# Kernel optimization log

Measured on AMD Instinct MI355X. Metric: run time of the kernel, lower is better.

Reference implementation:

```python
import jax, jax.numpy as jnp
import numpy as np

B, S, D, H = 4, 4096, 1024, 64


def setup_inputs() -> dict:
    key = jax.random.key(0)
    k1, k2, k3, k4 = jax.random.split(key, 4)
    x = jax.random.normal(k1, (B, S, D), dtype=jnp.float32)
    # nn.Linear(D, H, bias=False) weights, stored as [D, H] for x @ W
    scale = 1.0 / np.sqrt(D)
    Wk = jax.random.uniform(k2, (D, H), dtype=jnp.float32, minval=-scale, maxval=scale)
    Wq = jax.random.uniform(k3, (D, H), dtype=jnp.float32, minval=-scale, maxval=scale)
    Wv = jax.random.uniform(k4, (D, H), dtype=jnp.float32, minval=-scale, maxval=scale)
    return {"x": x, "Wq": Wq, "Wk": Wk, "Wv": Wv}


def reference(x, Wq, Wk, Wv):
    # x: [B, S, D]
    head_size = Wq.shape[-1]
    q = jnp.einsum('bsd,dh->bsh', x, Wq)
    k = jnp.einsum('bsd,dh->bsh', x, Wk)
    v = jnp.einsum('bsd,dh->bsh', x, Wv)
    scores = jnp.einsum('bqh,bkh->bqk', q, k) * (head_size ** -0.5)  # [B,S,S]
    S_ = x.shape[1]
    causal = jnp.tril(jnp.ones((S_, S_), dtype=bool))
    scores = jnp.where(causal[None, :, :], scores, -jnp.inf)
    attn = jax.nn.softmax(scores, axis=-1)
    return jnp.einsum('bqk,bkh->bqh', attn, v)  # [B,S,H]
```

## Files before the change

kernel.cpp:

```cpp
#include <hip/hip_runtime.h>

typedef __attribute__((ext_vector_type(8))) short bf16x8;
typedef __attribute__((ext_vector_type(4))) short bf16x4;
typedef __attribute__((ext_vector_type(4))) float f32x4;

#define MFMA16(A, Bv, C) __builtin_amdgcn_mfma_f32_16x16x32_bf16((A), (Bv), (C), 0, 0, 0)

static constexpr int NB = 4, NS = 4096, ND = 1024, NH = 64;

__device__ __forceinline__ unsigned short f2bf(float f) {
    union { float f; unsigned int u; } x; x.f = f;
    unsigned int r = x.u + 0x7fffu + ((x.u >> 16) & 1u);
    return (unsigned short)(r >> 16);
}

__device__ __forceinline__ void gload_lds16(const void* g, void* l) {
    __builtin_amdgcn_global_load_lds((const __attribute__((address_space(1))) void*)g,
                                     (__attribute__((address_space(3))) void*)l, 16, 0, 0);
}

__global__ __launch_bounds__(256) void wconv(
    const float* __restrict__ Wq, const float* __restrict__ Wk,
    const float* __restrict__ Wv, unsigned short* __restrict__ wT)
{
    int mn = blockIdx.x;
    int m = mn >> 6, n = mn & 63;
    const float* W = (m == 0) ? Wq : (m == 1) ? Wk : Wv;
    unsigned short* dst = wT + (size_t)mn * ND;
    for (int k = threadIdx.x; k < ND; k += 256)
        dst[k] = f2bf(W[(size_t)k * NH + n]);
}

__global__ __launch_bounds__(512) void qkv_proj(
    const float* __restrict__ x, const unsigned short* __restrict__ wT,
    unsigned short* __restrict__ qo, unsigned short* __restrict__ ko,
    unsigned short* __restrict__ vt)
{
    __shared__ unsigned short Ws[2][192][64];
    __shared__ unsigned short Xs[2][32][72];
    __shared__ unsigned short Ls[32][72];

    const int tid  = threadIdx.x;
    const int lane = tid & 63;
    const int w    = tid >> 6;
    const int lr   = lane & 15;
    const int lg   = lane >> 4;
    const int mg   = w >> 2;
    const int cg   = w & 3;
    const int mbase = blockIdx.x * 32;

    const int wr8 = lane >> 3;
    const int wck = (lane & 7) ^ wr8;
    const int xrow = tid & 31;
    const int xcg  = tid >> 5;

    f32x4 acc[3];
    #pragma unroll
    for (int f = 0; f < 3; ++f) acc[f] = (f32x4){0.f, 0.f, 0.f, 0.f};

    const float* xsrc = x + (size_t)(mbase + xrow) * ND + xcg * 4;

    #define STAGE_W(buf, kb)                                                         \
        do {                                                                         \
            _Pragma("unroll")                                                        \
            for (int i_ = 0; i_ < 3; ++i_) {                                         \
                int rb_ = w * 24 + i_ * 8;                                           \
                gload_lds16(wT + (size_t)(rb_ + wr8) * ND + (kb) + wck * 8,          \
                            &Ws[buf][rb_][0]);                                       \
            }                                                                        \
        } while (0)

    #define LOADX(kb) do { xr = *(const float4*)(xsrc + (kb)); } while (0)

    #define WRITEX(buf)                                                              \
        do {                                                                         \
            bf16x4 p_;                                                               \
            p_[0] = (short)f2bf(xr.x); p_[1] = (short)f2bf(xr.y);                    \
            p_[2] = (short)f2bf(xr.z); p_[3] = (short)f2bf(xr.w);                    \
            *(bf16x4*)&Xs[buf][xrow][xcg * 4] = p_;                                  \
        } while (0)

    float4 xr;
    STAGE_W(0, 0);
    LOADX(0);
    WRITEX(0);
    __syncthreads();

    for (int kt = 0; kt < 16; ++kt) {
        const int cur = kt & 1;
        if (kt + 1 < 16) {
            STAGE_W(cur ^ 1, (kt + 1) * 64);
            LOADX((kt + 1) * 64);
        }

        #pragma unroll
        for (int kk = 0; kk < 2; ++kk) {
            bf16x8 af = *(const bf16x8*)&Xs[cur][mg * 16 + lr][(kk * 4 + lg) * 8];
            #pragma unroll
            for (int f = 0; f < 3; ++f) {
                int row = cg * 48 + f * 16 + lr;
                bf16x8 bfr = *(const bf16x8*)&Ws[cur][row][((kk * 4 + lg) ^ (lr & 7)) * 8];
                acc[f] = MFMA16(af, bfr, acc[f]);
            }
        }

        if (kt + 1 < 16) WRITEX(cur ^ 1);
        __syncthreads();
    }

    #pragma unroll
    for (int f = 0; f < 3; ++f) {
        int b16 = cg * 3 + f;
        int sel = b16 >> 2;
        int col = (b16 & 3) * 16 + lr;
        #pragma unroll
        for (int rr = 0; rr < 4; ++rr) {
            int mrow = mg * 16 + lg * 4 + rr;
            float v = acc[f][rr];
            if (sel == 0)
                qo[(size_t)(mbase + mrow) * NH + col] = f2bf(v * 0.125f);
            else if (sel == 1)
                ko[(size_t)(mbase + mrow) * NH + col] = f2bf(v);
            else
                Ls[mrow][col] = f2bf(v);
        }
    }
    __syncthreads();
    {
        int h  = tid >> 3;
        int s4 = (tid & 7) * 4;
        bf16x4 v0;
        #pragma unroll
        for (int jj = 0; jj < 4; ++jj) v0[jj] = (short)Ls[s4 + jj][h];
        int b_ = mbase >> 12;
        int sb = (mbase & (NS - 1)) + s4;
        *(bf16x4*)(vt + ((size_t)(b_ * NH + h)) * NS + sb) = v0;
    }
    #undef STAGE_W
    #undef LOADX
    #undef WRITEX
}

__global__ __launch_bounds__(256) void attn_part(
    const unsigned short* __restrict__ q, const unsigned short* __restrict__ k,
    const unsigned short* __restrict__ vt, float* __restrict__ pO,
    float* __restrict__ pm, float* __restrict__ pl, float* __restrict__ out)
{
    __shared__ unsigned short Kt[2][64][64];
    __shared__ unsigned short Vt[2][64][64];
    __shared__ unsigned short Ps[4][16][72];

    const int bid = blockIdx.x;
    const int b = bid & 3;
    const int j = (bid >> 2) & 63;
    const int c = bid >> 8;
    if (c > (j >> 3)) return;
    const int nch = (j >> 3) + 1;
    const int ntile = (j + 1 - c * 8 < 8) ? (j + 1 - c * 8) : 8;
    const int tg0 = c * 8;

    const int tid  = threadIdx.x;
    const int lane = tid & 63;
    const int w    = tid >> 6;
    const int lr   = lane & 15;
    const int lg   = lane >> 4;
    const size_t bq = (size_t)b * NS;
    const int qb = j * 64;

    const int srow = lane >> 3;
    const int schk = (lane & 7) ^ srow;

    #define STAGEKV(buf, tg)                                                          \
        do {                                                                          \
            int kvb_ = (tg) * 64;                                                     \
            if (w < 2) {                                                              \
                _Pragma("unroll")                                                     \
                for (int i_ = 0; i_ < 4; ++i_) {                                      \
                    int rb_ = w * 32 + i_ * 8;                                        \
                    const unsigned short* src_ =                                      \
                        k + (bq + kvb_ + rb_ + srow) * NH + schk * 8;                 \
                    gload_lds16(src_, &Kt[buf][rb_][0]);                              \
                }                                                                     \
            } else {                                                                  \
                _Pragma("unroll")                                                     \
                for (int i_ = 0; i_ < 4; ++i_) {                                      \
                    int rb_ = (w - 2) * 32 + i_ * 8;                                  \
                    const unsigned short* src_ =                                      \
                        vt + ((size_t)(b * NH + rb_ + srow)) * NS + kvb_ + schk * 8;  \
                    gload_lds16(src_, &Vt[buf][rb_][0]);                              \
                }                                                                     \
            }                                                                         \
        } while (0)

    bf16x8 qf0, qf1;
    {
        const unsigned short* qp = q + (bq + qb + w * 16 + lr) * NH + lg * 8;
        qf0 = *(const bf16x8*)qp;
        qf1 = *(const bf16x8*)(qp + 32);
    }

    f32x4 O[4];
    #pragma unroll
    for (int i = 0; i < 4; ++i) O[i] = (f32x4){0.f, 0.f, 0.f, 0.f};
    float mrow = -3.0e38f, lsum = 0.f;

    STAGEKV(0, tg0);
    __syncthreads();

    int cur = 0;
    for (int t = 0; t < ntile; ++t) {
        const int tg = tg0 + t;
        STAGEKV(cur ^ 1, (t + 1 < ntile) ? tg + 1 : tg0);

        f32x4 sf[4];
        #pragma unroll
        for (int f = 0; f < 4; ++f) {
            f32x4 s = (f32x4){0.f, 0.f, 0.f, 0.f};
            int row = f * 16 + lr;
            bf16x8 kb0 = *(const bf16x8*)&Kt[cur][row][((lg    ) ^ (lr & 7)) * 8];
            bf16x8 kb1 = *(const bf16x8*)&Kt[cur][row][((lg + 4) ^ (lr & 7)) * 8];
            s = MFMA16(kb0, qf0, s);
            s = MFMA16(kb1, qf1, s);
            sf[f] = s;
        }

        if (tg == j) {
            #pragma unroll
            for (int f = 0; f < 4; ++f)
                #pragma unroll
                for (int r = 0; r < 4; ++r) {
                    int kvl = f * 16 + lg * 4 + r;
                    int ql  = w * 16 + lr;
                    if (kvl > ql) sf[f][r] = -3.0e38f;
                }
        }

        float pmx = fmaxf(fmaxf(fmaxf(sf[0][0], sf[0][1]), fmaxf(sf[0][2], sf[0][3])),
                          fmaxf(fmaxf(sf[1][0], sf[1][1]), fmaxf(sf[1][2], sf[1][3])));
        float pmx2 = fmaxf(fmaxf(fmaxf(sf[2][0], sf[2][1]), fmaxf(sf[2][2], sf[2][3])),
                           fmaxf(fmaxf(sf[3][0], sf[3][1]), fmaxf(sf[3][2], sf[3][3])));
        pmx = fmaxf(pmx, pmx2);
        pmx = fmaxf(pmx, __shfl_xor(pmx, 16));
        pmx = fmaxf(pmx, __shfl_xor(pmx, 32));
        float mnew = fmaxf(mrow, pmx);
        float corr = __expf(mrow - mnew);
        mrow = mnew;
        float rs = 0.f;
        #pragma unroll
        for (int f = 0; f < 4; ++f)
            #pragma unroll
            for (int r = 0; r < 4; ++r) {
                float p = __expf(sf[f][r] - mnew);
                sf[f][r] = p;
                rs += p;
            }
        rs += __shfl_xor(rs, 16);
        rs += __shfl_xor(rs, 32);
        lsum = lsum * corr + rs;
        #pragma unroll
        for (int hf = 0; hf < 4; ++hf) O[hf] *= corr;

        #pragma unroll
        for (int f = 0; f < 4; ++f)
            #pragma unroll
            for (int r = 0; r < 4; ++r)
                Ps[w][lr][f * 16 + lg * 4 + r] = f2bf(sf[f][r]);

        bf16x8 pb0 = *(const bf16x8*)&Ps[w][lr][lg * 8];
        bf16x8 pb1 = *(const bf16x8*)&Ps[w][lr][32 + lg * 8];

        #pragma unroll
        for (int hf = 0; hf < 4; ++hf) {
            int row = hf * 16 + lr;
            bf16x8 vb0 = *(const bf16x8*)&Vt[cur][row][((lg    ) ^ (lr & 7)) * 8];
            bf16x8 vb1 = *(const bf16x8*)&Vt[cur][row][((lg + 4) ^ (lr & 7)) * 8];
            O[hf] = MFMA16(vb0, pb0, O[hf]);
            O[hf] = MFMA16(vb1, pb1, O[hf]);
        }

        __syncthreads();
        cur ^= 1;
    }

    if (nch == 1) {
        float inv = 1.f / lsum;
        float* op = out + (bq + qb + w * 16 + lr) * NH;
        #pragma unroll
        for (int hf = 0; hf < 4; ++hf) {
            f32x4 o = O[hf] * inv;
            *(f32x4*)&op[hf * 16 + lg * 4] = o;
        }
        return;
    }

    const int a8 = j >> 3, r8 = j & 7;
    const int pidx = b * 288 + (a8 + 1) * (4 * a8 + r8) + c;
    float* Po = pO + (size_t)pidx * 4096;
    #pragma unroll
    for (int hf = 0; hf < 4; ++hf)
        *(f32x4*)&Po[(w * 16 + lr) * 64 + hf * 16 + lg * 4] = O[hf];
    if (lane < 16) {
        pm[pidx * 64 + w * 16 + lane] = mrow;
        pl[pidx * 64 + w * 16 + lane] = lsum;
    }
    #undef STAGEKV
}

__global__ __launch_bounds__(256) void attn_merge(
    const float* __restrict__ pO, const float* __restrict__ pm,
    const float* __restrict__ pl, float* __restrict__ out)
{
    const int bid = blockIdx.x;
    const int b = bid & 3, j = 8 + (bid >> 2);
    const int nch = (j >> 3) + 1;
    const int a8 = j >> 3, r8 = j & 7;
    const int pbase = b * 288 + (a8 + 1) * (4 * a8 + r8);
    const int tid = threadIdx.x;
    const int row = tid >> 2, hq = (tid & 3) * 16;

    float M = -3.0e38f, L = 0.f;
    f32x4 acc0 = {0,0,0,0}, acc1 = {0,0,0,0}, acc2 = {0,0,0,0}, acc3 = {0,0,0,0};
    for (int cc = 0; cc < nch; ++cc) {
        int pidx = pbase + cc;
        float mc = pm[pidx * 64 + row];
        float lc = pl[pidx * 64 + row];
        const f32x4* po = (const f32x4*)(pO + (size_t)pidx * 4096 + row * 64 + hq);
        float Mn = fmaxf(M, mc);
        float sO = __expf(M - Mn), sN = __expf(mc - Mn);
        L = L * sO + lc * sN;
        acc0 = acc0 * sO + po[0] * sN;
        acc1 = acc1 * sO + po[1] * sN;
        acc2 = acc2 * sO + po[2] * sN;
        acc3 = acc3 * sO + po[3] * sN;
        M = Mn;
    }
    float inv = 1.f / L;
    float* op = out + ((size_t)b * NS + (size_t)j * 64 + row) * NH + hq;
    *(f32x4*)(op + 0)  = acc0 * inv;
    *(f32x4*)(op + 4)  = acc1 * inv;
    *(f32x4*)(op + 8)  = acc2 * inv;
    *(f32x4*)(op + 12) = acc3 * inv;
}

extern "C" void kernel_launch(void* const* d_in, const int* in_sizes, int n_in,
                              void* d_out, int out_size, void* d_ws, size_t ws_size,
                              hipStream_t stream)
{
    const float* x  = (const float*)d_in[0];
    const float* Wq = (const float*)d_in[1];
    const float* Wk = (const float*)d_in[2];
    const float* Wv = (const float*)d_in[3];
    float* out = (float*)d_out;

    const size_t n = (size_t)NB * NS * NH;
    unsigned short* qb_ = (unsigned short*)d_ws;
    unsigned short* kb_ = qb_ + n;
    unsigned short* vT  = kb_ + n;
    unsigned short* wT  = vT + n;
    float* pO  = (float*)(wT + 192 * 1024);
    float* pm_ = pO + (size_t)1152 * 4096;
    float* pl_ = pm_ + 1152 * 64;

    wconv<<<dim3(192), dim3(256), 0, stream>>>(Wq, Wk, Wv, wT);
    qkv_proj<<<dim3(512), dim3(512), 0, stream>>>(x, wT, qb_, kb_, vT);
    attn_part<<<dim3(2048), dim3(256), 0, stream>>>(qb_, kb_, vT, pO, pm_, pl_, out);
    attn_merge<<<dim3(224), dim3(256), 0, stream>>>(pO, pm_, pl_, out);
}
```

Baseline: 64.06 us.

## Double query tile to 128 rows per attention block with 8 waves

The attention partial kernel now gives each block a 128-row query tile with 512 threads (8 waves) instead of 64 rows with 4 waves. Each staged K/V tile in LDS is therefore shared by twice as many query rows, which halves the K/V global traffic and the number of blocks and partial results. The causal mask now covers the last two KV tiles, and the merge kernel and workspace layout are rescaled to match. The cost is coarser work granularity, fewer blocks for load balancing, and more wasted masked work on the diagonal.

```diff
diff --git a/kernel.cpp b/kernel.cpp
--- a/kernel.cpp
+++ b/kernel.cpp
@@ -141,22 +141,23 @@
     #undef WRITEX
 }
 
-__global__ __launch_bounds__(256) void attn_part(
+__global__ __launch_bounds__(512) void attn_part(
     const unsigned short* __restrict__ q, const unsigned short* __restrict__ k,
     const unsigned short* __restrict__ vt, float* __restrict__ pO,
     float* __restrict__ pm, float* __restrict__ pl, float* __restrict__ out)
 {
     __shared__ unsigned short Kt[2][64][64];
     __shared__ unsigned short Vt[2][64][64];
-    __shared__ unsigned short Ps[4][16][72];
+    __shared__ unsigned short Ps[8][16][72];
 
     const int bid = blockIdx.x;
     const int b = bid & 3;
-    const int j = (bid >> 2) & 63;
-    const int c = bid >> 8;
-    if (c > (j >> 3)) return;
-    const int nch = (j >> 3) + 1;
-    const int ntile = (j + 1 - c * 8 < 8) ? (j + 1 - c * 8) : 8;
+    const int J = (bid >> 2) & 31;
+    const int c = bid >> 7;
+    const int nch = (J + 4) >> 2;
+    if (c >= nch) return;
+    const int T = 2 * (J + 1);
+    const int ntile = (T - c * 8 < 8) ? (T - c * 8) : 8;
     const int tg0 = c * 8;
 
     const int tid  = threadIdx.x;
@@ -165,7 +166,7 @@
     const int lr   = lane & 15;
     const int lg   = lane >> 4;
     const size_t bq = (size_t)b * NS;
-    const int qb = j * 64;
+    const int qb = J * 128;
 
     const int srow = lane >> 3;
     const int schk = (lane & 7) ^ srow;
@@ -173,18 +174,18 @@
     #define STAGEKV(buf, tg)                                                          \
         do {                                                                          \
             int kvb_ = (tg) * 64;                                                     \
-            if (w < 2) {                                                              \
+            if (w < 4) {                                                              \
                 _Pragma("unroll")                                                     \
-                for (int i_ = 0; i_ < 4; ++i_) {                                      \
-                    int rb_ = w * 32 + i_ * 8;                                        \
+                for (int i_ = 0; i_ < 2; ++i_) {                                      \
+                    int rb_ = w * 16 + i_ * 8;                                        \
                     const unsigned short* src_ =                                      \
                         k + (bq + kvb_ + rb_ + srow) * NH + schk * 8;                 \
                     gload_lds16(src_, &Kt[buf][rb_][0]);                              \
                 }                                                                     \
             } else {                                                                  \
                 _Pragma("unroll")                                                     \
-                for (int i_ = 0; i_ < 4; ++i_) {                                      \
-                    int rb_ = (w - 2) * 32 + i_ * 8;                                  \
+                for (int i_ = 0; i_ < 2; ++i_) {                                      \
+                    int rb_ = (w - 4) * 16 + i_ * 8;                                  \
                     const unsigned short* src_ =                                      \
                         vt + ((size_t)(b * NH + rb_ + srow)) * NS + kvb_ + schk * 8;  \
                     gload_lds16(src_, &Vt[buf][rb_][0]);                              \
@@ -224,13 +225,13 @@
             sf[f] = s;
         }
 
-        if (tg == j) {
+        if (tg >= 2 * J) {
+            const int ql = qb + w * 16 + lr;
             #pragma unroll
             for (int f = 0; f < 4; ++f)
                 #pragma unroll
                 for (int r = 0; r < 4; ++r) {
-                    int kvl = f * 16 + lg * 4 + r;
-                    int ql  = w * 16 + lr;
+                    int kvl = tg * 64 + f * 16 + lg * 4 + r;
                     if (kvl > ql) sf[f][r] = -3.0e38f;
                 }
         }
@@ -293,28 +294,28 @@
         return;
     }
 
-    const int a8 = j >> 3, r8 = j & 7;
-    const int pidx = b * 288 + (a8 + 1) * (4 * a8 + r8) + c;
-    float* Po = pO + (size_t)pidx * 4096;
+    const int a4 = J >> 2, r4 = J & 3;
+    const int pidx = b * 144 + (a4 + 1) * (2 * a4 + r4) + c;
+    float* Po = pO + (size_t)pidx * 8192;
     #pragma unroll
     for (int hf = 0; hf < 4; ++hf)
         *(f32x4*)&Po[(w * 16 + lr) * 64 + hf * 16 + lg * 4] = O[hf];
     if (lane < 16) {
-        pm[pidx * 64 + w * 16 + lane] = mrow;
-        pl[pidx * 64 + w * 16 + lane] = lsum;
+        pm[pidx * 128 + w * 16 + lane] = mrow;
+        pl[pidx * 128 + w * 16 + lane] = lsum;
     }
     #undef STAGEKV
 }
 
-__global__ __launch_bounds__(256) void attn_merge(
+__global__ __launch_bounds__(512) void attn_merge(
     const float* __restrict__ pO, const float* __restrict__ pm,
     const float* __restrict__ pl, float* __restrict__ out)
 {
     const int bid = blockIdx.x;
-    const int b = bid & 3, j = 8 + (bid >> 2);
-    const int nch = (j >> 3) + 1;
-    const int a8 = j >> 3, r8 = j & 7;
-    const int pbase = b * 288 + (a8 + 1) * (4 * a8 + r8);
+    const int b = bid & 3, J = 4 + (bid >> 2);
+    const int nch = (J + 4) >> 2;
+    const int a4 = J >> 2, r4 = J & 3;
+    const int pbase = b * 144 + (a4 + 1) * (2 * a4 + r4);
     const int tid = threadIdx.x;
     const int row = tid >> 2, hq = (tid & 3) * 16;
 
@@ -322,9 +323,9 @@
     f32x4 acc0 = {0,0,0,0}, acc1 = {0,0,0,0}, acc2 = {0,0,0,0}, acc3 = {0,0,0,0};
     for (int cc = 0; cc < nch; ++cc) {
         int pidx = pbase + cc;
-        float mc = pm[pidx * 64 + row];
-        float lc = pl[pidx * 64 + row];
-        const f32x4* po = (const f32x4*)(pO + (size_t)pidx * 4096 + row * 64 + hq);
+        float mc = pm[pidx * 128 + row];
+        float lc = pl[pidx * 128 + row];
+        const f32x4* po = (const f32x4*)(pO + (size_t)pidx * 8192 + row * 64 + hq);
         float Mn = fmaxf(M, mc);
         float sO = __expf(M - Mn), sN = __expf(mc - Mn);
         L = L * sO + lc * sN;
@@ -335,7 +336,7 @@
         M = Mn;
     }
     float inv = 1.f / L;
-    float* op = out + ((size_t)b * NS + (size_t)j * 64 + row) * NH + hq;
+    float* op = out + ((size_t)b * NS + (size_t)J * 128 + row) * NH + hq;
     *(f32x4*)(op + 0)  = acc0 * inv;
     *(f32x4*)(op + 4)  = acc1 * inv;
     *(f32x4*)(op + 8)  = acc2 * inv;
@@ -358,11 +359,11 @@
     unsigned short* vT  = kb_ + n;
     unsigned short* wT  = vT + n;
     float* pO  = (float*)(wT + 192 * 1024);
-    float* pm_ = pO + (size_t)1152 * 4096;
-    float* pl_ = pm_ + 1152 * 64;
+    float* pm_ = pO + (size_t)576 * 8192;
+    float* pl_ = pm_ + 576 * 128;
 
     wconv<<<dim3(192), dim3(256), 0, stream>>>(Wq, Wk, Wv, wT);
     qkv_proj<<<dim3(512), dim3(512), 0, stream>>>(x, wT, qb_, kb_, vT);
-    attn_part<<<dim3(2048), dim3(256), 0, stream>>>(qb_, kb_, vT, pO, pm_, pl_, out);
-    attn_merge<<<dim3(224), dim3(256), 0, stream>>>(pO, pm_, pl_, out);
-}
+    attn_part<<<dim3(1024), dim3(512), 0, stream>>>(qb_, kb_, vT, pO, pm_, pl_, out);
+    attn_merge<<<dim3(112), dim3(512), 0, stream>>>(pO, pm_, pl_, out);
+}
```

New measurement: 64.90 us. No clear change (+1.3%).
